# Optimization experiments

Hardware: AMD Instinct MI355X
Metric: run time of the kernel (lower is better)

## Reference

```python
import jax, jax.numpy as jnp
import numpy as np
from jax import lax

N = 100000   # num_nodes
E = 1600000  # num_edges (avg degree 16)
F = 128      # num_features
H = 256      # hidden_channels
C = 64       # num_classes
K = 10       # propagation steps
ALPHA = 0.1
BETA = 0.5
THETA = 0.5
EPS = 1e-5   # BatchNorm eps


def setup_inputs() -> dict:
    key = jax.random.key(0)
    ks = jax.random.split(key, 16)
    x = jax.random.normal(ks[0], (N, F), dtype=jnp.float32)
    src = jax.random.randint(ks[1], (E,), 0, N, dtype=jnp.int32)
    dst = jax.random.randint(ks[2], (E,), 0, N, dtype=jnp.int32)
    # row-normalized adjacency weights so repeated A@z stays bounded
    deg = jax.ops.segment_sum(jnp.ones((E,), jnp.float32), dst, num_segments=N)
    w = (1.0 / jnp.maximum(deg, 1.0))[dst]
    # MLP params (Linear + BatchNorm per hidden layer)
    W1 = jax.random.normal(ks[3], (F, H), dtype=jnp.float32) * 0.05
    b1 = jnp.zeros((H,), jnp.float32)
    g1 = jnp.ones((H,), jnp.float32)
    be1 = jnp.zeros((H,), jnp.float32)
    W2 = jax.random.normal(ks[4], (H, H), dtype=jnp.float32) * 0.05
    b2 = jnp.zeros((H,), jnp.float32)
    g2 = jnp.ones((H,), jnp.float32)
    be2 = jnp.zeros((H,), jnp.float32)
    W3 = jax.random.normal(ks[5], (H, C), dtype=jnp.float32) * 0.05
    b3 = jnp.zeros((C,), jnp.float32)
    # lazy caches (warm-start memories); nonzero so the blend branch is taken
    z_sam = jax.random.normal(ks[6], (N, C), dtype=jnp.float32) * 0.1
    g_sam = jax.random.normal(ks[7], (N, C), dtype=jnp.float32) * 0.01
    return dict(x=x, src=src, dst=dst, w=w,
                W1=W1, b1=b1, g1=g1, be1=be1,
                W2=W2, b2=b2, g2=g2, be2=be2,
                W3=W3, b3=b3, z_sam=z_sam, g_sam=g_sam, size=N)


def _bn(h, gamma, beta):
    # BatchNorm1d in training mode: batch statistics over nodes
    mu = jnp.mean(h, axis=0)
    var = jnp.var(h, axis=0)
    return (h - mu) * jax.lax.rsqrt(var + EPS) * gamma + beta


def reference(x, src, dst, w, W1, b1, g1, be1, W2, b2, g2, be2, W3, b3,
              z_sam, g_sam, size):
    # MLP stack: Linear -> BN -> ReLU (dropout omitted: deterministic reference)
    h = jax.nn.relu(_bn(x @ W1 + b1, g1, be1))
    h = jax.nn.relu(_bn(h @ W2 + b2, g2, be2))
    logits = h @ W3 + b3  # [N, C]

    def spmm(z):
        # (A @ z)_i = sum_{j -> i} w_ij * z_j
        return jax.ops.segment_sum(z[src] * w[:, None], dst, num_segments=N)

    # Lazy_Prop.forward: warm-start blend, then K propagation steps
    use_x = jnp.all(z_sam[:size] == 0.0)
    z0 = jnp.where(use_x, logits, (1.0 - BETA) * z_sam + BETA * logits)
    z = lax.fori_loop(0, K, lambda i, z: (1.0 - ALPHA) * spmm(z) + ALPHA * logits, z0)
    return jax.nn.log_softmax(z, axis=1)
```

## Files before the change

### kernel.cpp

```cpp
#include <hip/hip_runtime.h>
#include <hip/hip_bf16.h>

#define NODES 100000
#define EDGES 1600000
#define FEAT  128
#define HID   256
#define CLS   64
#define KPROP 10
#define ALPHA_C 0.1f
#define BETA_C  0.5f
#define BN_EPS  1e-5f

typedef __attribute__((ext_vector_type(8))) short short8;
typedef __attribute__((ext_vector_type(4))) float f32x4;

static __device__ __forceinline__ unsigned short f2b(float f) {
    __hip_bfloat16 h = __float2bfloat16(f);
    return *(unsigned short*)&h;
}
static __device__ __forceinline__ float b2f(unsigned short u) {
    __hip_bfloat16 h;
    *(unsigned short*)&h = u;
    return __bfloat162float(h);
}
static __device__ __forceinline__ float asf(unsigned int u) {
    union { unsigned int u; float f; } c; c.u = u; return c.f;
}

__global__ void packwt_k(const float* __restrict__ W, unsigned short* __restrict__ Wt,
                         int K, int N)
{
    int i = blockIdx.x * 256 + threadIdx.x;
    if (i < K * N) {
        int k = i / N, n = i - k * N;
        Wt[(size_t)n * K + k] = f2b(W[i]);
    }
}

template<bool AF32, bool FUSE, bool STATS, bool OUTF32, int KK, int NCOLG>
__global__ __launch_bounds__(256, 2)
void gemm_lds_k(const void* __restrict__ Ain, const unsigned short* __restrict__ Wt,
                const float* __restrict__ bias,
                const float* __restrict__ scale, const float* __restrict__ shift,
                void* __restrict__ outp,
                float* __restrict__ gsum, float* __restrict__ gsq,
                int M, int N, int nchunks, int nblk)
{
    constexpr int NK8 = KK / 32;
    __shared__ unsigned short Blds[64 * KK];
    __shared__ float Slds[KK];
    __shared__ float Hlds[KK];

    const int lane = threadIdx.x & 63;
    const int wv   = threadIdx.x >> 6;
    const int quad = lane >> 4;
    const int l16  = lane & 15;
    const int colg = (NCOLG > 1) ? (blockIdx.x % NCOLG) : 0;
    const int blk0 = (NCOLG > 1) ? (blockIdx.x / NCOLG) : blockIdx.x;
    const int colbase = colg * 64;

    {
        const unsigned short* wp = Wt + (size_t)colbase * KK;
        constexpr int ELEMS = 64 * KK / 8;
        #pragma unroll
        for (int i0 = 0; i0 < ELEMS; i0 += 256) {
            int i  = i0 + threadIdx.x;
            int c  = i / (KK / 8);
            int k8 = i - c * (KK / 8);
            short8 v = *(const short8*)(wp + (size_t)c * KK + k8 * 8);
            int byte = c * (KK * 2) + ((k8 * 16) ^ ((c & 7) << 4));
            *(short8*)((char*)Blds + byte) = v;
        }
        if constexpr (FUSE) {
            for (int i = threadIdx.x; i < KK; i += 256) {
                Slds[i] = scale[i];
                Hlds[i] = shift[i];
            }
        }
    }
    __syncthreads();

    float bcol[4];
    #pragma unroll
    for (int ct = 0; ct < 4; ++ct) bcol[ct] = bias[colbase + ct * 16 + l16];

    float ps[4] = {0.f, 0.f, 0.f, 0.f};
    float pq[4] = {0.f, 0.f, 0.f, 0.f};

    float4 af0[2][AF32 ? NK8 : 1][2];
    float4 af1[2][AF32 ? NK8 : 1][2];
    short8 ah0[2][AF32 ? 1 : NK8];
    short8 ah1[2][AF32 ? 1 : NK8];

#define LOAD_A(AF, AH, CHK)                                                    \
    if ((CHK) < nchunks) {                                                     \
        const int rb_ = (CHK) * 128 + wv * 32;                                 \
        _Pragma("unroll")                                                      \
        for (int rt = 0; rt < 2; ++rt) {                                       \
            const int row_ = rb_ + rt * 16 + l16;                              \
            const bool ok_ = row_ < M;                                         \
            if constexpr (AF32) {                                              \
                const float* ap_ = (const float*)Ain + (size_t)row_ * KK + quad * 8; \
                _Pragma("unroll")                                              \
                for (int ks = 0; ks < NK8; ++ks) {                             \
                    AF[rt][ks][0] = ok_ ? *(const float4*)(ap_ + ks * 32)                \
                                        : (float4){0.f, 0.f, 0.f, 0.f};        \
                    AF[rt][ks][1] = ok_ ? *(const float4*)(ap_ + ks * 32 + 4)            \
                                        : (float4){0.f, 0.f, 0.f, 0.f};        \
                }                                                              \
            } else {                                                           \
                const unsigned short* ap_ = (const unsigned short*)Ain + (size_t)row_ * KK + quad * 8; \
                _Pragma("unroll")                                              \
                for (int ks = 0; ks < NK8; ++ks)                               \
                    AH[rt][ks] = ok_ ? *(const short8*)(ap_ + ks * 32)         \
                                     : (short8){0, 0, 0, 0, 0, 0, 0, 0};       \
            }                                                                  \
        }                                                                      \
    }

#define COMPUTE(AF, AH, CHK)                                                   \
    {                                                                          \
        const int rb_ = (CHK) * 128 + wv * 32;                                 \
        f32x4 acc[2][4];                                                       \
        _Pragma("unroll")                                                      \
        for (int i = 0; i < 2; ++i)                                            \
            _Pragma("unroll")                                                  \
            for (int j = 0; j < 4; ++j)                                        \
                acc[i][j] = (f32x4){0.f, 0.f, 0.f, 0.f};                       \
        _Pragma("unroll")                                                      \
        for (int ks = 0; ks < NK8; ++ks) {                                     \
            const int k_ = ks * 32 + quad * 8;                                 \
            float sc[8], sh[8];                                                \
            if constexpr (FUSE) {                                              \
                float4 s0 = *(const float4*)&Slds[k_];                         \
                float4 s1 = *(const float4*)&Slds[k_ + 4];                     \
                float4 h0 = *(const float4*)&Hlds[k_];                         \
                float4 h1 = *(const float4*)&Hlds[k_ + 4];                     \
                sc[0]=s0.x; sc[1]=s0.y; sc[2]=s0.z; sc[3]=s0.w;                \
                sc[4]=s1.x; sc[5]=s1.y; sc[6]=s1.z; sc[7]=s1.w;                \
                sh[0]=h0.x; sh[1]=h0.y; sh[2]=h0.z; sh[3]=h0.w;                \
                sh[4]=h1.x; sh[5]=h1.y; sh[6]=h1.z; sh[7]=h1.w;                \
            }                                                                  \
            short8 a2[2];                                                      \
            _Pragma("unroll")                                                  \
            for (int rt = 0; rt < 2; ++rt) {                                   \
                float v[8];                                                    \
                if constexpr (AF32) {                                          \
                    float4 t0 = AF[rt][ks][0];                                 \
                    float4 t1 = AF[rt][ks][1];                                 \
                    v[0]=t0.x; v[1]=t0.y; v[2]=t0.z; v[3]=t0.w;                \
                    v[4]=t1.x; v[5]=t1.y; v[6]=t1.z; v[7]=t1.w;                \
                } else {                                                       \
                    _Pragma("unroll")                                          \
                    for (int j = 0; j < 8; ++j)                                \
                        v[j] = b2f((unsigned short)AH[rt][ks][j]);             \
                }                                                              \
                if constexpr (FUSE) {                                          \
                    _Pragma("unroll")                                          \
                    for (int j = 0; j < 8; ++j)                                \
                        v[j] = fmaxf(fmaf(v[j], sc[j], sh[j]), 0.f);           \
                }                                                              \
                short8 av;                                                     \
                _Pragma("unroll")                                              \
                for (int j = 0; j < 8; ++j) av[j] = (short)f2b(v[j]);          \
                a2[rt] = av;                                                   \
            }                                                                  \
            _Pragma("unroll")                                                  \
            for (int ct = 0; ct < 4; ++ct) {                                   \
                const int boff = (ct * 16 + l16) * (KK * 2)                    \
                               + ((ks * 64 + quad * 16) ^ ((l16 & 7) << 4));   \
                short8 bf = *(const short8*)((const char*)Blds + boff);        \
                acc[0][ct] = __builtin_amdgcn_mfma_f32_16x16x32_bf16(a2[0], bf, acc[0][ct], 0, 0, 0); \
                acc[1][ct] = __builtin_amdgcn_mfma_f32_16x16x32_bf16(a2[1], bf, acc[1][ct], 0, 0, 0); \
            }                                                                  \
        }                                                                      \
        _Pragma("unroll")                                                      \
        for (int ct = 0; ct < 4; ++ct) {                                       \
            const int col_ = colbase + ct * 16 + l16;                          \
            _Pragma("unroll")                                                  \
            for (int rt = 0; rt < 2; ++rt) {                                   \
                _Pragma("unroll")                                              \
                for (int r2 = 0; r2 < 4; ++r2) {                               \
                    const int row_ = rb_ + rt * 16 + quad * 4 + r2;            \
                    if (row_ < M) {                                            \
                        float vv = acc[rt][ct][r2] + bcol[ct];                 \
                        if constexpr (STATS) { ps[ct] += vv; pq[ct] += vv * vv; } \
                        if constexpr (OUTF32) {                                \
                            ((float*)outp)[(size_t)row_ * N + col_] = vv;      \
                        } else {                                               \
                            ((unsigned short*)outp)[(size_t)row_ * N + col_] = f2b(vv); \
                        }                                                      \
                    }                                                          \
                }                                                              \
            }                                                                  \
        }                                                                      \
    }

    int chunk = blk0;
    LOAD_A(af0, ah0, chunk)
    while (chunk < nchunks) {
        const int cn1 = chunk + nblk;
        LOAD_A(af1, ah1, cn1)
        __builtin_amdgcn_sched_barrier(0);
        COMPUTE(af0, ah0, chunk)
        chunk = cn1;
        if (chunk >= nchunks) break;
        const int cn2 = chunk + nblk;
        LOAD_A(af0, ah0, cn2)
        __builtin_amdgcn_sched_barrier(0);
        COMPUTE(af1, ah1, chunk)
        chunk = cn2;
    }
#undef LOAD_A
#undef COMPUTE

    if constexpr (STATS) {
        #pragma unroll
        for (int ct = 0; ct < 4; ++ct) {
            float s = ps[ct];
            s += __shfl_xor(s, 16, 64);
            s += __shfl_xor(s, 32, 64);
            float q = pq[ct];
            q += __shfl_xor(q, 16, 64);
            q += __shfl_xor(q, 32, 64);
            if (lane < 16) {
                atomicAdd(&gsum[colbase + ct * 16 + lane], s);
                atomicAdd(&gsq[colbase + ct * 16 + lane], q);
            }
        }
    }
}

__global__ void bnfin_k(const float* __restrict__ sum, const float* __restrict__ sq,
                        const float* __restrict__ g, const float* __restrict__ be,
                        float* __restrict__ scale, float* __restrict__ shift)
{
    int c = threadIdx.x;
    float mu = sum[c] * (1.f / NODES);
    float var = sq[c] * (1.f / NODES) - mu * mu;
    float sc = g[c] * rsqrtf(var + BN_EPS);
    scale[c] = sc;
    shift[c] = be[c] - mu * sc;
}

__global__ void flag_k(const float* __restrict__ zs, int* __restrict__ flag)
{
    int i = blockIdx.x * 256 + threadIdx.x;
    bool nz = (i < NODES * CLS) && (zs[i] != 0.f);
    if (__any(nz)) {
        if ((threadIdx.x & 63) == 0) *flag = 1;
    }
}

__global__ void blend_k(const float* __restrict__ zs, const float* __restrict__ logits,
                        const int* __restrict__ flag, unsigned short* __restrict__ z0)
{
    int i = blockIdx.x * 256 + threadIdx.x;
    if (i < NODES * CLS) {
        float l = logits[i];
        float v = (*flag) ? ((1.f - BETA_C) * zs[i] + BETA_C * l) : l;
        z0[i] = f2b(v);
    }
}

__global__ void count_k(const int* __restrict__ dst, int* __restrict__ cnt, int T)
{
    int t = blockIdx.x * 256 + threadIdx.x;
    #pragma unroll
    for (int u = 0; u < 8; ++u) {
        int e = t + u * T;
        int d = (e < EDGES) ? dst[e] : NODES;
        atomicAdd(&cnt[d], 1);
    }
}

__global__ void scan1_k(const int* __restrict__ cnt, int* __restrict__ rowptr,
                        int* __restrict__ bsum)
{
    __shared__ int s[256];
    int tid = threadIdx.x;
    int i = blockIdx.x * 256 + tid;
    int v = (i < NODES) ? cnt[i] : 0;
    s[tid] = v;
    __syncthreads();
    for (int off = 1; off < 256; off <<= 1) {
        int t = (tid >= off) ? s[tid - off] : 0;
        __syncthreads();
        s[tid] += t;
        __syncthreads();
    }
    if (i < NODES) rowptr[i] = s[tid] - v;
    if (tid == 255) bsum[blockIdx.x] = s[255];
}

__global__ void scan2_k(const int* __restrict__ bsum, int* __restrict__ boffs, int nb)
{
    __shared__ int s[512];
    int tid = threadIdx.x;
    int v = (tid < nb) ? bsum[tid] : 0;
    s[tid] = v;
    __syncthreads();
    for (int off = 1; off < 512; off <<= 1) {
        int t = (tid >= off) ? s[tid - off] : 0;
        __syncthreads();
        s[tid] += t;
        __syncthreads();
    }
    if (tid < nb) boffs[tid] = s[tid] - v;
}

__global__ void scan3_k(int* __restrict__ rowptr, const int* __restrict__ boffs,
                        int* __restrict__ cursor)
{
    int i = blockIdx.x * 256 + threadIdx.x;
    if (i < NODES) {
        int v = rowptr[i] + boffs[blockIdx.x];
        rowptr[i] = v;
        cursor[i] = v;
    }
    if (i == 0) rowptr[NODES] = EDGES;
}

__global__ void fill_k(const int* __restrict__ src, const int* __restrict__ dst,
                       int* __restrict__ cursor, int* __restrict__ esrc, int T)
{
    int t = blockIdx.x * 256 + threadIdx.x;
    int e[8], d[8], s[8], p[8];
    bool ok[8];
    #pragma unroll
    for (int u = 0; u < 8; ++u) {
        e[u] = t + u * T;
        ok[u] = e[u] < EDGES;
        d[u] = ok[u] ? dst[e[u]] : NODES;
        s[u] = ok[u] ? src[e[u]] : 0;
    }
    #pragma unroll
    for (int u = 0; u < 8; ++u)
        p[u] = atomicAdd(&cursor[d[u]], 1);
    #pragma unroll
    for (int u = 0; u < 8; ++u)
        if (ok[u]) esrc[p[u]] = s[u];
}

__global__ __launch_bounds__(256)
void prop_k(const int* __restrict__ rowptr, const int* __restrict__ esrc,
            const unsigned long long* __restrict__ zin, const float* __restrict__ logits,
            unsigned long long* __restrict__ zout)
{
    int row = blockIdx.x * 16 + (threadIdx.x >> 4);
    if (row >= NODES) return;
    int l16 = threadIdx.x & 15;
    int beg = rowptr[row], end = rowptr[row + 1];
    float a0 = 0.f, a1 = 0.f, a2 = 0.f, a3 = 0.f;

    for (int cbeg = beg; cbeg < end; cbeg += 16) {
        int e = cbeg + l16;
        int s_l = (e < end) ? esrc[e] : 0;
        int cnt = min(16, end - cbeg);
        int j = 0;
        for (; j + 8 <= cnt; j += 8) {
            int idx[8];
            #pragma unroll
            for (int u = 0; u < 8; ++u) idx[u] = __shfl(s_l, j + u, 16);
            unsigned long long vv[8];
            #pragma unroll
            for (int u = 0; u < 8; ++u)
                vv[u] = __hip_atomic_load(zin + (size_t)idx[u] * 16 + l16,
                                          __ATOMIC_RELAXED, __HIP_MEMORY_SCOPE_AGENT);
            #pragma unroll
            for (int u = 0; u < 8; ++u) {
                unsigned int lo = (unsigned int)vv[u];
                unsigned int hi = (unsigned int)(vv[u] >> 32);
                a0 += asf(lo << 16);
                a1 += asf(lo & 0xffff0000u);
                a2 += asf(hi << 16);
                a3 += asf(hi & 0xffff0000u);
            }
        }
        for (; j < cnt; ++j) {
            int s0 = __shfl(s_l, j, 16);
            unsigned long long v = __hip_atomic_load(zin + (size_t)s0 * 16 + l16,
                                                     __ATOMIC_RELAXED, __HIP_MEMORY_SCOPE_AGENT);
            unsigned int lo = (unsigned int)v;
            unsigned int hi = (unsigned int)(v >> 32);
            a0 += asf(lo << 16);
            a1 += asf(lo & 0xffff0000u);
            a2 += asf(hi << 16);
            a3 += asf(hi & 0xffff0000u);
        }
    }
    float dg = (float)(end - beg);
    float inv = 1.f / fmaxf(dg, 1.f);
    float4 lv = *(const float4*)(logits + (size_t)row * CLS + l16 * 4);
    float cc = (1.f - ALPHA_C) * inv;
    float r0 = cc * a0 + ALPHA_C * lv.x;
    float r1 = cc * a1 + ALPHA_C * lv.y;
    float r2 = cc * a2 + ALPHA_C * lv.z;
    float r3 = cc * a3 + ALPHA_C * lv.w;
    unsigned int w0 = ((unsigned int)f2b(r1) << 16) | (unsigned int)f2b(r0);
    unsigned int w1 = ((unsigned int)f2b(r3) << 16) | (unsigned int)f2b(r2);
    zout[(size_t)row * 16 + l16] = ((unsigned long long)w1 << 32) | w0;
}

__global__ __launch_bounds__(256)
void logsoftmax_k(const unsigned short* __restrict__ z, float* __restrict__ out)
{
    int row = blockIdx.x * 4 + (threadIdx.x >> 6);
    if (row >= NODES) return;
    int lane = threadIdx.x & 63;
    float v = b2f(z[(size_t)row * CLS + lane]);
    float m = v;
    #pragma unroll
    for (int off = 32; off > 0; off >>= 1) m = fmaxf(m, __shfl_xor(m, off, 64));
    float ex = expf(v - m);
    float s = ex;
    #pragma unroll
    for (int off = 32; off > 0; off >>= 1) s += __shfl_xor(s, off, 64);
    out[(size_t)row * CLS + lane] = (v - m) - logf(s);
}

extern "C" void kernel_launch(void* const* d_in, const int* in_sizes, int n_in,
                              void* d_out, int out_size, void* d_ws, size_t ws_size,
                              hipStream_t stream)
{
    const float* x   = (const float*)d_in[0];
    const int*   src = (const int*)d_in[1];
    const int*   dst = (const int*)d_in[2];
    const float* W1  = (const float*)d_in[4];
    const float* b1  = (const float*)d_in[5];
    const float* g1  = (const float*)d_in[6];
    const float* be1 = (const float*)d_in[7];
    const float* W2  = (const float*)d_in[8];
    const float* b2  = (const float*)d_in[9];
    const float* g2  = (const float*)d_in[10];
    const float* be2 = (const float*)d_in[11];
    const float* W3  = (const float*)d_in[12];
    const float* b3  = (const float*)d_in[13];
    const float* zsam = (const float*)d_in[14];
    float* outp = (float*)d_out;

    uint8_t* base = (uint8_t*)d_ws;
    float* s_scale1 = (float*)(base);
    float* s_shift1 = s_scale1 + 256;
    float* s_scale2 = s_shift1 + 256;
    float* s_shift2 = s_scale2 + 256;
    float* s_sum    = s_shift2 + 256;
    float* s_sq     = s_sum + 256;
    int*   flag     = (int*)(s_sq + 256);

    unsigned short* Wt1 = (unsigned short*)(base + (1 << 14));
    unsigned short* Wt2 = Wt1 + (size_t)FEAT * HID;
    unsigned short* Wt3 = Wt2 + (size_t)HID * HID;
    unsigned short* h1  = Wt3 + (size_t)HID * CLS;
    unsigned short* h2  = h1 + (size_t)NODES * HID;
    float* logits = (float*)(h2 + (size_t)NODES * HID);
    unsigned short* zA  = (unsigned short*)(logits + (size_t)NODES * CLS);
    unsigned short* zB  = zA + (size_t)NODES * CLS;
    int* esrc   = (int*)(zB + (size_t)NODES * CLS);
    int* rowptr = esrc + EDGES;
    int* cursor = rowptr + (NODES + 1);
    int* cnt    = cursor + (NODES + 1);
    int* bsum   = cnt + (NODES + 1);
    int* boffs  = bsum + 512;

    const int NCHUNK = (NODES + 127) / 128;
    const int NBLK   = (NCHUNK + 1) / 2;
    const int SCANB  = (NODES + 255) / 256;
    const int EB8    = (EDGES / 8 + 255) / 256;
    const int ET8    = EB8 * 256;

    packwt_k<<<(FEAT * HID + 255) / 256, 256, 0, stream>>>(W1, Wt1, FEAT, HID);
    packwt_k<<<(HID * HID + 255) / 256, 256, 0, stream>>>(W2, Wt2, HID, HID);
    packwt_k<<<(HID * CLS + 255) / 256, 256, 0, stream>>>(W3, Wt3, HID, CLS);

    hipMemsetAsync(cnt, 0, (NODES + 1) * sizeof(int), stream);
    count_k<<<EB8, 256, 0, stream>>>(dst, cnt, ET8);
    scan1_k<<<SCANB, 256, 0, stream>>>(cnt, rowptr, bsum);
    scan2_k<<<1, 512, 0, stream>>>(bsum, boffs, SCANB);
    scan3_k<<<SCANB, 256, 0, stream>>>(rowptr, boffs, cursor);
    fill_k<<<EB8, 256, 0, stream>>>(src, dst, cursor, esrc, ET8);

    hipMemsetAsync(s_sum, 0, 512 * sizeof(float), stream);
    gemm_lds_k<true, false, true, false, FEAT, 4><<<NBLK * 4, 256, 0, stream>>>(
        x, Wt1, b1, nullptr, nullptr, h1, s_sum, s_sq, NODES, HID, NCHUNK, NBLK);
    bnfin_k<<<1, 256, 0, stream>>>(s_sum, s_sq, g1, be1, s_scale1, s_shift1);

    hipMemsetAsync(s_sum, 0, 512 * sizeof(float), stream);
    gemm_lds_k<false, true, true, false, HID, 4><<<NBLK * 4, 256, 0, stream>>>(
        h1, Wt2, b2, s_scale1, s_shift1, h2, s_sum, s_sq, NODES, HID, NCHUNK, NBLK);
    bnfin_k<<<1, 256, 0, stream>>>(s_sum, s_sq, g2, be2, s_scale2, s_shift2);

    gemm_lds_k<false, true, false, true, HID, 1><<<NBLK, 256, 0, stream>>>(
        h2, Wt3, b3, s_scale2, s_shift2, logits, nullptr, nullptr, NODES, CLS, NCHUNK, NBLK);

    hipMemsetAsync(flag, 0, sizeof(int), stream);
    flag_k<<<(NODES * CLS + 255) / 256, 256, 0, stream>>>(zsam, flag);
    blend_k<<<(NODES * CLS + 255) / 256, 256, 0, stream>>>(zsam, logits, flag, zA);

    const int PROPB = (NODES + 15) / 16;
    for (int it = 0; it < KPROP; ++it) {
        const unsigned long long* zi = (const unsigned long long*)((it & 1) ? zB : zA);
        unsigned long long* zo = (unsigned long long*)((it & 1) ? zA : zB);
        prop_k<<<PROPB, 256, 0, stream>>>(rowptr, esrc, zi, logits, zo);
    }

    logsoftmax_k<<<(NODES + 3) / 4, 256, 0, stream>>>(zA, outp);
}
```

Baseline: 953.0 us.

## Privatize CSR build atomics into 8 replicas and unroll full 16-edge chunks

The counting and fill phases of the CSR build now spread their atomics over 8 replicated counter/cursor arrays chosen by block index. A new kernel prefix-sums the replicas per node so that each replica owns a disjoint sub-range of the row. Edge indices are read as int4 vectors. This is meant to reduce atomic contention on hot counters, at the cost of extra memory traffic for the 8x arrays. Separately, the propagation kernel gets a fully unrolled 16-load path for full chunks to raise memory-level parallelism.

```diff
diff --git a/kernel.cpp b/kernel.cpp
--- a/kernel.cpp
+++ b/kernel.cpp
@@ -263,15 +263,33 @@
     }
 }
 
-__global__ void count_k(const int* __restrict__ dst, int* __restrict__ cnt, int T)
+__global__ void count_k(const int* __restrict__ dst, int* __restrict__ cntx)
 {
     int t = blockIdx.x * 256 + threadIdx.x;
+    if (t >= EDGES / 4) return;
+    int4 d = ((const int4*)dst)[t];
+    int* c = cntx + (size_t)(blockIdx.x & 7) * NODES;
+    atomicAdd(&c[d.x], 1);
+    atomicAdd(&c[d.y], 1);
+    atomicAdd(&c[d.z], 1);
+    atomicAdd(&c[d.w], 1);
+}
+
+__global__ void sumoff_k(int* __restrict__ cntx, int* __restrict__ cnt)
+{
+    int n = blockIdx.x * 256 + threadIdx.x;
+    if (n >= NODES) return;
+    int tot = 0;
+    int p[8];
     #pragma unroll
-    for (int u = 0; u < 8; ++u) {
-        int e = t + u * T;
-        int d = (e < EDGES) ? dst[e] : NODES;
-        atomicAdd(&cnt[d], 1);
-    }
+    for (int x = 0; x < 8; ++x) {
+        p[x] = tot;
+        tot += cntx[(size_t)x * NODES + n];
+    }
+    #pragma unroll
+    for (int x = 0; x < 8; ++x)
+        cntx[(size_t)x * NODES + n] = p[x];
+    cnt[n] = tot;
 }
 
 __global__ void scan1_k(const int* __restrict__ cnt, int* __restrict__ rowptr,
@@ -310,36 +328,35 @@
 }
 
 __global__ void scan3_k(int* __restrict__ rowptr, const int* __restrict__ boffs,
-                        int* __restrict__ cursor)
+                        const int* __restrict__ cntx, int* __restrict__ curx)
 {
     int i = blockIdx.x * 256 + threadIdx.x;
     if (i < NODES) {
         int v = rowptr[i] + boffs[blockIdx.x];
         rowptr[i] = v;
-        cursor[i] = v;
+        #pragma unroll
+        for (int x = 0; x < 8; ++x)
+            curx[(size_t)x * NODES + i] = v + cntx[(size_t)x * NODES + i];
     }
     if (i == 0) rowptr[NODES] = EDGES;
 }
 
 __global__ void fill_k(const int* __restrict__ src, const int* __restrict__ dst,
-                       int* __restrict__ cursor, int* __restrict__ esrc, int T)
+                       int* __restrict__ curx, int* __restrict__ esrc)
 {
     int t = blockIdx.x * 256 + threadIdx.x;
-    int e[8], d[8], s[8], p[8];
-    bool ok[8];
-    #pragma unroll
-    for (int u = 0; u < 8; ++u) {
-        e[u] = t + u * T;
-        ok[u] = e[u] < EDGES;
-        d[u] = ok[u] ? dst[e[u]] : NODES;
-        s[u] = ok[u] ? src[e[u]] : 0;
-    }
-    #pragma unroll
-    for (int u = 0; u < 8; ++u)
-        p[u] = atomicAdd(&cursor[d[u]], 1);
-    #pragma unroll
-    for (int u = 0; u < 8; ++u)
-        if (ok[u]) esrc[p[u]] = s[u];
+    if (t >= EDGES / 4) return;
+    int4 d = ((const int4*)dst)[t];
+    int4 s = ((const int4*)src)[t];
+    int* cur = curx + (size_t)(blockIdx.x & 7) * NODES;
+    int p0 = atomicAdd(&cur[d.x], 1);
+    int p1 = atomicAdd(&cur[d.y], 1);
+    int p2 = atomicAdd(&cur[d.z], 1);
+    int p3 = atomicAdd(&cur[d.w], 1);
+    esrc[p0] = s.x;
+    esrc[p1] = s.y;
+    esrc[p2] = s.z;
+    esrc[p3] = s.w;
 }
 
 __global__ __launch_bounds__(256)
@@ -357,18 +374,17 @@
         int e = cbeg + l16;
         int s_l = (e < end) ? esrc[e] : 0;
         int cnt = min(16, end - cbeg);
-        int j = 0;
-        for (; j + 8 <= cnt; j += 8) {
-            int idx[8];
+        if (cnt == 16) {
+            int idx[16];
             #pragma unroll
-            for (int u = 0; u < 8; ++u) idx[u] = __shfl(s_l, j + u, 16);
-            unsigned long long vv[8];
+            for (int u = 0; u < 16; ++u) idx[u] = __shfl(s_l, u, 16);
+            unsigned long long vv[16];
             #pragma unroll
-            for (int u = 0; u < 8; ++u)
+            for (int u = 0; u < 16; ++u)
                 vv[u] = __hip_atomic_load(zin + (size_t)idx[u] * 16 + l16,
                                           __ATOMIC_RELAXED, __HIP_MEMORY_SCOPE_AGENT);
             #pragma unroll
-            for (int u = 0; u < 8; ++u) {
+            for (int u = 0; u < 16; ++u) {
                 unsigned int lo = (unsigned int)vv[u];
                 unsigned int hi = (unsigned int)(vv[u] >> 32);
                 a0 += asf(lo << 16);
@@ -376,17 +392,38 @@
                 a2 += asf(hi << 16);
                 a3 += asf(hi & 0xffff0000u);
             }
-        }
-        for (; j < cnt; ++j) {
-            int s0 = __shfl(s_l, j, 16);
-            unsigned long long v = __hip_atomic_load(zin + (size_t)s0 * 16 + l16,
-                                                     __ATOMIC_RELAXED, __HIP_MEMORY_SCOPE_AGENT);
-            unsigned int lo = (unsigned int)v;
-            unsigned int hi = (unsigned int)(v >> 32);
-            a0 += asf(lo << 16);
-            a1 += asf(lo & 0xffff0000u);
-            a2 += asf(hi << 16);
-            a3 += asf(hi & 0xffff0000u);
+        } else {
+            int j = 0;
+            for (; j + 8 <= cnt; j += 8) {
+                int idx[8];
+                #pragma unroll
+                for (int u = 0; u < 8; ++u) idx[u] = __shfl(s_l, j + u, 16);
+                unsigned long long vv[8];
+                #pragma unroll
+                for (int u = 0; u < 8; ++u)
+                    vv[u] = __hip_atomic_load(zin + (size_t)idx[u] * 16 + l16,
+                                              __ATOMIC_RELAXED, __HIP_MEMORY_SCOPE_AGENT);
+                #pragma unroll
+                for (int u = 0; u < 8; ++u) {
+                    unsigned int lo = (unsigned int)vv[u];
+                    unsigned int hi = (unsigned int)(vv[u] >> 32);
+                    a0 += asf(lo << 16);
+                    a1 += asf(lo & 0xffff0000u);
+                    a2 += asf(hi << 16);
+                    a3 += asf(hi & 0xffff0000u);
+                }
+            }
+            for (; j < cnt; ++j) {
+                int s0 = __shfl(s_l, j, 16);
+                unsigned long long v = __hip_atomic_load(zin + (size_t)s0 * 16 + l16,
+                                                         __ATOMIC_RELAXED, __HIP_MEMORY_SCOPE_AGENT);
+                unsigned int lo = (unsigned int)v;
+                unsigned int hi = (unsigned int)(v >> 32);
+                a0 += asf(lo << 16);
+                a1 += asf(lo & 0xffff0000u);
+                a2 += asf(hi << 16);
+                a3 += asf(hi & 0xffff0000u);
+            }
         }
     }
     float dg = (float)(end - beg);
@@ -457,28 +494,29 @@
     unsigned short* zA  = (unsigned short*)(logits + (size_t)NODES * CLS);
     unsigned short* zB  = zA + (size_t)NODES * CLS;
     int* esrc   = (int*)(zB + (size_t)NODES * CLS);
-    int* rowptr = esrc + EDGES;
-    int* cursor = rowptr + (NODES + 1);
-    int* cnt    = cursor + (NODES + 1);
-    int* bsum   = cnt + (NODES + 1);
+    int* cntx   = esrc + EDGES;
+    int* curx   = cntx + (size_t)8 * NODES;
+    int* rowptr = curx + (size_t)8 * NODES;
+    int* cnt    = rowptr + (NODES + 1);
+    int* bsum   = cnt + NODES;
     int* boffs  = bsum + 512;
 
     const int NCHUNK = (NODES + 127) / 128;
     const int NBLK   = (NCHUNK + 1) / 2;
     const int SCANB  = (NODES + 255) / 256;
-    const int EB8    = (EDGES / 8 + 255) / 256;
-    const int ET8    = EB8 * 256;
+    const int EB4    = (EDGES / 4 + 255) / 256;
 
     packwt_k<<<(FEAT * HID + 255) / 256, 256, 0, stream>>>(W1, Wt1, FEAT, HID);
     packwt_k<<<(HID * HID + 255) / 256, 256, 0, stream>>>(W2, Wt2, HID, HID);
     packwt_k<<<(HID * CLS + 255) / 256, 256, 0, stream>>>(W3, Wt3, HID, CLS);
 
-    hipMemsetAsync(cnt, 0, (NODES + 1) * sizeof(int), stream);
-    count_k<<<EB8, 256, 0, stream>>>(dst, cnt, ET8);
+    hipMemsetAsync(cntx, 0, (size_t)8 * NODES * sizeof(int), stream);
+    count_k<<<EB4, 256, 0, stream>>>(dst, cntx);
+    sumoff_k<<<SCANB, 256, 0, stream>>>(cntx, cnt);
     scan1_k<<<SCANB, 256, 0, stream>>>(cnt, rowptr, bsum);
     scan2_k<<<1, 512, 0, stream>>>(bsum, boffs, SCANB);
-    scan3_k<<<SCANB, 256, 0, stream>>>(rowptr, boffs, cursor);
-    fill_k<<<EB8, 256, 0, stream>>>(src, dst, cursor, esrc, ET8);
+    scan3_k<<<SCANB, 256, 0, stream>>>(rowptr, boffs, cntx, curx);
+    fill_k<<<EB4, 256, 0, stream>>>(src, dst, curx, esrc);
 
     hipMemsetAsync(s_sum, 0, 512 * sizeof(float), stream);
     gemm_lds_k<true, false, true, false, FEAT, 4><<<NBLK * 4, 256, 0, stream>>>(
```

After: 905.7 us. -5.0%, faster.
